# Performance work log

Measured on AMD Instinct MI355X. Metric: run time of the kernel, lower is better.

The kernel has to match this reference:

```python
import jax, jax.numpy as jnp
import numpy as np

EMBED_DIM = 1024
NUM_HEADS = 16
HEAD_DIM = EMBED_DIM // NUM_HEADS
CONSTANT = 1.0
EPS = 1e-4


def setup_inputs() -> dict:
    key = jax.random.key(0)
    ks = jax.random.split(key, 9)
    L, N, E = 2048, 4, EMBED_DIM
    scale = 1.0 / np.sqrt(E)
    return {
        "query": jax.random.normal(ks[0], (L, N, E), jnp.float32),
        "key": jax.random.normal(ks[1], (L, N, E), jnp.float32),
        "value": jax.random.normal(ks[2], (L, N, E), jnp.float32),
        "Wq": jax.random.normal(ks[3], (E, E), jnp.float32) * scale,
        "bq": jnp.zeros((E,), jnp.float32),
        "Wk": jax.random.normal(ks[4], (E, E), jnp.float32) * scale,
        "bk": jnp.zeros((E,), jnp.float32),
        "Wv": jax.random.normal(ks[5], (E, E), jnp.float32) * scale,
        "bv": jnp.zeros((E,), jnp.float32),
    }


def reference(query, key, value, Wq, bq, Wk, bk, Wv, bv):
    tgt_len, bsz, E = query.shape
    src_len = key.shape[0]
    h, d = NUM_HEADS, HEAD_DIM

    # Linear projections (nn.Linear: x @ W.T + b)
    q = query @ Wq.T + bq
    k = key @ Wk.T + bk
    v = value @ Wv.T + bv

    # (L, N, E) -> (N*h, L, d)
    def split_heads(x, slen):
        return x.reshape(slen, bsz * h, d).transpose(1, 0, 2)

    q = jax.nn.relu(split_heads(q, tgt_len))
    k = jax.nn.relu(split_heads(k, src_len))
    v = split_heads(v, src_len)

    # sin/cos positional reweighting: idx = pi/2 * arange(1, m+1) * constant / m
    m = max(src_len, tgt_len)
    idx = (np.pi / 2) * jnp.arange(1, m + 1, dtype=q.dtype) * CONSTANT / m  # (m,)
    sin_w = jnp.sin(idx)[None, :, None]  # (1, m, 1)
    cos_w = jnp.cos(idx)[None, :, None]

    q_ = jnp.concatenate([q * sin_w[:, :tgt_len], q * cos_w[:, :tgt_len]], axis=-1)  # (n, L, 2d)
    k_ = jnp.concatenate([k * sin_w[:, :src_len], k * cos_w[:, :src_len]], axis=-1)  # (n, S, 2d)

    # Non-causal linear attention: O(N) in sequence length
    kv_ = jnp.einsum('nld,nlm->ndm', k_, v)                       # (n, 2d, d)
    z_ = 1.0 / jnp.clip(jnp.einsum('nld,nd->nl', q_, k_.sum(axis=1)), EPS, None)  # (n, L)
    attn_output = jnp.einsum('nld,ndm,nl->nlm', q_, kv_, z_)      # (n, L, d)

    # (N*h, L, d) -> (L, N, E)
    attn_output = attn_output.transpose(1, 0, 2).reshape(tgt_len, bsz, E)
    return attn_output
```

## Files before the change

kernel.cpp:

```cpp
#include <hip/hip_runtime.h>
#include <cstdint>

#define L_SEQ 2048
#define NB 4
#define EMB 1024
#define NHEAD 16
#define HD 64
#define M_ROWS (L_SEQ * NB)
#define ANGC (1.5707963267948966f / 2048.0f)
#define NSPLIT 16
#define XN ((size_t)M_ROWS * EMB)
#define WN ((size_t)EMB * EMB)
#define NX16 (1 << 19)
#define NW16 (1 << 16)

typedef __bf16 bf16x8 __attribute__((ext_vector_type(8)));
typedef float f32x4 __attribute__((ext_vector_type(4)));
typedef unsigned short u16x8 __attribute__((ext_vector_type(8)));

__device__ __forceinline__ unsigned short f2bf(float f) {
  unsigned int u = __float_as_uint(f);
  u += 0x7fffu + ((u >> 16) & 1u);
  return (unsigned short)(u >> 16);
}
__device__ __forceinline__ float bf2f(unsigned short u) {
  return __uint_as_float((unsigned int)u << 16);
}

__device__ __forceinline__ void gload_lds16(const void* g, void* l) {
  __builtin_amdgcn_global_load_lds(
      (const __attribute__((address_space(1))) void*)g,
      (__attribute__((address_space(3))) void*)l, 16, 0, 0);
}

__global__ __launch_bounds__(256) void cvt_all_kernel(
    const float* __restrict__ q, const float* __restrict__ k,
    const float* __restrict__ v, const float* __restrict__ wq,
    const float* __restrict__ wk, const float* __restrict__ wv,
    unsigned short* __restrict__ xb, unsigned short* __restrict__ wb) {
  int i = blockIdx.x * 256 + threadIdx.x;
  const float* src;
  unsigned short* dst;
  size_t off;
  if (i < 3 * NX16) {
    int sel = i >> 19;
    off = (size_t)(i & (NX16 - 1));
    src = (sel == 0) ? q : (sel == 1) ? k : v;
    dst = xb + (size_t)sel * XN;
  } else {
    int j = i - 3 * NX16;
    int sel = j >> 16;
    off = (size_t)(j & (NW16 - 1));
    src = (sel == 0) ? wq : (sel == 1) ? wk : wv;
    dst = wb + (size_t)sel * WN;
  }
  const float4* s4 = (const float4*)src + off * 4;
  float4 a = s4[0], b = s4[1], c = s4[2], d = s4[3];
  union { unsigned short u[8]; uint4 vv; } o0, o1;
  o0.u[0] = f2bf(a.x); o0.u[1] = f2bf(a.y); o0.u[2] = f2bf(a.z); o0.u[3] = f2bf(a.w);
  o0.u[4] = f2bf(b.x); o0.u[5] = f2bf(b.y); o0.u[6] = f2bf(b.z); o0.u[7] = f2bf(b.w);
  o1.u[0] = f2bf(c.x); o1.u[1] = f2bf(c.y); o1.u[2] = f2bf(c.z); o1.u[3] = f2bf(c.w);
  o1.u[4] = f2bf(d.x); o1.u[5] = f2bf(d.y); o1.u[6] = f2bf(d.z); o1.u[7] = f2bf(d.w);
  uint4* d4 = (uint4*)(dst + off * 16);
  d4[0] = o0.vv;
  d4[1] = o1.vv;
}

__global__ __launch_bounds__(256) void proj_gemm_kernel(
    const unsigned short* __restrict__ Xall, const unsigned short* __restrict__ Wall,
    const float* __restrict__ b0, const float* __restrict__ b1,
    const float* __restrict__ b2, unsigned short* __restrict__ Pall) {
  const int which = blockIdx.z;
  const unsigned short* Xb = Xall + (size_t)which * XN;
  const unsigned short* Wb = Wall + (size_t)which * WN;
  const float* bias = (which == 0) ? b0 : (which == 1) ? b1 : b2;
  unsigned short* outp = Pall + (size_t)which * XN;
  const bool relu = (which < 2);
  const int bm0 = blockIdx.x * 128;
  const int bn0 = blockIdx.y * 128;

  __shared__ unsigned short As[2][128 * 32];
  __shared__ unsigned short Bs[2][128 * 32];

  const int tid = threadIdx.x;
  const int lane = tid & 63, wave = tid >> 6;
  const int wrow = (wave >> 1) * 64, wcol = (wave & 1) * 64;
  const int fr = lane & 15, fk = lane >> 4;

  f32x4 acc[4][4];
#pragma unroll
  for (int m = 0; m < 4; ++m)
#pragma unroll
    for (int n = 0; n < 4; ++n) acc[m][n] = (f32x4){0.f, 0.f, 0.f, 0.f};

  auto stage = [&](int kt, int buf) {
#pragma unroll
    for (int i = 0; i < 2; ++i) {
      int c = i * 256 + wave * 64 + lane;
      int row = c >> 2;
      int kgs = (c & 3) ^ ((row >> 1) & 3);
      int ldsoff = (i * 256 + wave * 64) * 16;
      gload_lds16(Xb + (size_t)(bm0 + row) * EMB + kt * 32 + kgs * 8,
                  (char*)&As[buf][0] + ldsoff);
      gload_lds16(Wb + (size_t)(bn0 + row) * EMB + kt * 32 + kgs * 8,
                  (char*)&Bs[buf][0] + ldsoff);
    }
  };

  stage(0, 0);
  __syncthreads();
  const int NK = EMB / 32;
  for (int kt = 0; kt < NK; ++kt) {
    int buf = kt & 1;
    if (kt + 1 < NK) stage(kt + 1, buf ^ 1);
    bf16x8 af[4], bfr[4];
#pragma unroll
    for (int m = 0; m < 4; ++m) {
      int row = wrow + m * 16 + fr;
      af[m] = *(const bf16x8*)((const char*)&As[buf][0] + row * 64 +
                               ((fk ^ ((row >> 1) & 3)) * 16));
    }
#pragma unroll
    for (int n = 0; n < 4; ++n) {
      int row = wcol + n * 16 + fr;
      bfr[n] = *(const bf16x8*)((const char*)&Bs[buf][0] + row * 64 +
                                ((fk ^ ((row >> 1) & 3)) * 16));
    }
#pragma unroll
    for (int m = 0; m < 4; ++m)
#pragma unroll
      for (int n = 0; n < 4; ++n)
        acc[m][n] = __builtin_amdgcn_mfma_f32_16x16x32_bf16(af[m], bfr[n],
                                                            acc[m][n], 0, 0, 0);
    __syncthreads();
  }

#pragma unroll
  for (int n = 0; n < 4; ++n) {
    int gc = bn0 + wcol + n * 16 + fr;
    float bv = bias[gc];
#pragma unroll
    for (int m = 0; m < 4; ++m) {
#pragma unroll
      for (int r = 0; r < 4; ++r) {
        int gr = bm0 + wrow + m * 16 + fk * 4 + r;
        float v = acc[m][n][r] + bv;
        if (relu) v = fmaxf(v, 0.f);
        outp[(size_t)gr * EMB + gc] = f2bf(v);
      }
    }
  }
}

__global__ __launch_bounds__(256) void kv_part_kernel(
    const unsigned short* __restrict__ kp, const unsigned short* __restrict__ vp,
    float* __restrict__ kvpart, float* __restrict__ kspart) {
  const int n = blockIdx.y;
  const int s = blockIdx.x;
  const int nb = n >> 4, head = n & 15;
  const int l0 = s * (L_SEQ / NSPLIT);
  __shared__ float kt[32][64];
  __shared__ float vt[32][64];
  __shared__ float wt[2][32];
  const int t = threadIdx.x;
  const int dg = t >> 3, mg = t & 7;

  float acc[4][8];
#pragma unroll
  for (int a = 0; a < 4; ++a)
#pragma unroll
    for (int b = 0; b < 8; ++b) acc[a][b] = 0.f;
  float ks[4] = {0.f, 0.f, 0.f, 0.f};

  for (int lt = l0; lt < l0 + (L_SEQ / NSPLIT); lt += 32) {
    {
      int i = t >> 3, c8 = (t & 7) * 8;
      u16x8 gk8 = *(const u16x8*)(kp + (size_t)((lt + i) * NB + nb) * EMB +
                                  head * HD + c8);
      u16x8 gv8 = *(const u16x8*)(vp + (size_t)((lt + i) * NB + nb) * EMB +
                                  head * HD + c8);
      float4 ka = {bf2f(gk8[0]), bf2f(gk8[1]), bf2f(gk8[2]), bf2f(gk8[3])};
      float4 kb = {bf2f(gk8[4]), bf2f(gk8[5]), bf2f(gk8[6]), bf2f(gk8[7])};
      float4 va = {bf2f(gv8[0]), bf2f(gv8[1]), bf2f(gv8[2]), bf2f(gv8[3])};
      float4 vb = {bf2f(gv8[4]), bf2f(gv8[5]), bf2f(gv8[6]), bf2f(gv8[7])};
      *(float4*)&kt[i][c8] = ka;
      *(float4*)&kt[i][c8 + 4] = kb;
      *(float4*)&vt[i][c8] = va;
      *(float4*)&vt[i][c8 + 4] = vb;
    }
    if (t < 32) {
      float ang = ANGC * (float)(lt + t + 1);
      wt[0][t] = __sinf(ang);
      wt[1][t] = __cosf(ang);
    }
    __syncthreads();
#pragma unroll 4
    for (int i = 0; i < 32; ++i) {
      float w = wt[dg >> 4][i];
      float4 kk4 = *(const float4*)&kt[i][(dg & 15) * 4];
      float kk[4];
      kk[0] = fmaxf(kk4.x, 0.f) * w; kk[1] = fmaxf(kk4.y, 0.f) * w;
      kk[2] = fmaxf(kk4.z, 0.f) * w; kk[3] = fmaxf(kk4.w, 0.f) * w;
      float4 v0 = *(const float4*)&vt[i][mg * 8];
      float4 v1 = *(const float4*)&vt[i][mg * 8 + 4];
      float vv[8] = {v0.x, v0.y, v0.z, v0.w, v1.x, v1.y, v1.z, v1.w};
#pragma unroll
      for (int a = 0; a < 4; ++a) {
#pragma unroll
        for (int b = 0; b < 8; ++b) acc[a][b] += kk[a] * vv[b];
        ks[a] += kk[a];
      }
    }
    __syncthreads();
  }

  float* kvn = kvpart + ((size_t)(s * 64 + n) * 128 + dg * 4) * 64 + mg * 8;
#pragma unroll
  for (int a = 0; a < 4; ++a) {
    *(float4*)&kvn[(size_t)a * 64 + 0] = *(float4*)&acc[a][0];
    *(float4*)&kvn[(size_t)a * 64 + 4] = *(float4*)&acc[a][4];
  }
  if (mg == 0) {
#pragma unroll
    for (int a = 0; a < 4; ++a)
      kspart[(size_t)(s * 64 + n) * 128 + dg * 4 + a] = ks[a];
  }
}

__global__ __launch_bounds__(256) void kv_reduce_kernel(
    const float* __restrict__ kvpart, const float* __restrict__ kspart,
    unsigned short* __restrict__ kvT, float* __restrict__ ksum) {
  const int b = blockIdx.x;
  const int n = b >> 2, mseg = b & 3;
  const int t = threadIdx.x;
  __shared__ float kvsum[128][17];

#pragma unroll
  for (int j = 0; j < 2; ++j) {
    int f4 = j * 256 + t;
    int dd = f4 >> 2, mm = f4 & 3;
    f32x4 s = (f32x4){0, 0, 0, 0};
#pragma unroll
    for (int p = 0; p < NSPLIT; ++p)
      s += *(const f32x4*)(kvpart + ((size_t)(p * 64 + n) * 128 + dd) * 64 +
                           mseg * 16 + mm * 4);
    kvsum[dd][mm * 4 + 0] = s[0];
    kvsum[dd][mm * 4 + 1] = s[1];
    kvsum[dd][mm * 4 + 2] = s[2];
    kvsum[dd][mm * 4 + 3] = s[3];
  }
  if (mseg == 0 && t < 128) {
    float s = 0.f;
#pragma unroll
    for (int p = 0; p < NSPLIT; ++p) s += kspart[(size_t)(p * 64 + n) * 128 + t];
    ksum[n * 128 + t] = s;
  }
  __syncthreads();

  int mloc = t >> 4, dd0 = (t & 15) * 8;
  union { unsigned short u[8]; uint4 vv; } o;
#pragma unroll
  for (int e = 0; e < 8; ++e) o.u[e] = f2bf(kvsum[dd0 + e][mloc]);
  *(uint4*)(kvT + ((size_t)n * 64 + mseg * 16 + mloc) * 128 + dd0) = o.vv;
}

__global__ __launch_bounds__(256) void out_mfma_kernel(
    const unsigned short* __restrict__ qp, const unsigned short* __restrict__ kvT,
    const float* __restrict__ ksum, float* __restrict__ out) {
  const int n = blockIdx.y;
  const int nb = n >> 4, head = n & 15;
  const int L0 = blockIdx.x * 64;
  const int t = threadIdx.x;
  const int lane = t & 63, wave = t >> 6;
  const int fr = lane & 15, fk = lane >> 4;

  __shared__ unsigned short q_lds[64 * 128];
  __shared__ unsigned short kvt_lds[64 * 128];
  __shared__ float ks_lds[128];
  __shared__ float z_lds[64];

  {
    int j = t >> 2, d0 = (t & 3) * 16;
    float ang = ANGC * (float)(L0 + j + 1);
    float sw = __sinf(ang), cw = __cosf(ang);
    const unsigned short* gq =
        qp + (size_t)((L0 + j) * NB + nb) * EMB + head * HD + d0;
    u16x8 qa = *(const u16x8*)gq;
    u16x8 qb = *(const u16x8*)(gq + 8);
    union { unsigned short u[8]; uint4 vv; } s0, s1, c0, c1;
#pragma unroll
    for (int e = 0; e < 8; ++e) {
      float fa = fmaxf(bf2f(qa[e]), 0.f);
      float fb = fmaxf(bf2f(qb[e]), 0.f);
      s0.u[e] = f2bf(fa * sw); s1.u[e] = f2bf(fb * sw);
      c0.u[e] = f2bf(fa * cw); c1.u[e] = f2bf(fb * cw);
    }
    int gs = (t & 3) * 2;
    *(uint4*)&q_lds[(j * 16 + ((gs + 0) ^ (j & 7))) * 8] = s0.vv;
    *(uint4*)&q_lds[(j * 16 + ((gs + 1) ^ (j & 7))) * 8] = s1.vv;
    *(uint4*)&q_lds[(j * 16 + ((gs + 8) ^ (j & 7))) * 8] = c0.vv;
    *(uint4*)&q_lds[(j * 16 + ((gs + 9) ^ (j & 7))) * 8] = c1.vv;
  }
  {
#pragma unroll
    for (int c = 0; c < 4; ++c) {
      int gi = t * 4 + c;
      int m = gi >> 4, g = gi & 15;
      uint4 v = *(const uint4*)(kvT + (size_t)n * 8192 + m * 128 + g * 8);
      *(uint4*)&kvt_lds[(m * 16 + (g ^ (m & 7))) * 8] = v;
    }
  }
  if (t < 128) ks_lds[t] = ksum[n * 128 + t];
  __syncthreads();

  {
    int row = t >> 2, seg = t & 3;
    float sum = 0.f;
#pragma unroll
    for (int g8 = 0; g8 < 4; ++g8) {
      int g = seg * 4 + g8;
      const unsigned short* qg = &q_lds[(row * 16 + (g ^ (row & 7))) * 8];
      u16x8 qv = *(const u16x8*)qg;
#pragma unroll
      for (int e = 0; e < 8; ++e) sum += bf2f(qv[e]) * ks_lds[g * 8 + e];
    }
    sum += __shfl_xor(sum, 1);
    sum += __shfl_xor(sum, 2);
    if (seg == 0) z_lds[row] = 1.f / fmaxf(sum, 1e-4f);
  }

  const int wrow = wave * 16;
  f32x4 acc[4];
#pragma unroll
  for (int nt = 0; nt < 4; ++nt) acc[nt] = (f32x4){0, 0, 0, 0};
#pragma unroll
  for (int kk = 0; kk < 4; ++kk) {
    int arow = wrow + fr;
    bf16x8 af = *(const bf16x8*)&q_lds[(arow * 16 + ((kk * 4 + fk) ^ (arow & 7))) * 8];
#pragma unroll
    for (int nt = 0; nt < 4; ++nt) {
      int brow = nt * 16 + fr;
      bf16x8 bf =
          *(const bf16x8*)&kvt_lds[(brow * 16 + ((kk * 4 + fk) ^ (brow & 7))) * 8];
      acc[nt] = __builtin_amdgcn_mfma_f32_16x16x32_bf16(af, bf, acc[nt], 0, 0, 0);
    }
  }

#pragma unroll
  for (int nt = 0; nt < 4; ++nt) {
#pragma unroll
    for (int r = 0; r < 4; ++r) {
      int lrow = wrow + fk * 4 + r;
      int m = nt * 16 + fr;
      out[((size_t)(L0 + lrow) * NB + nb) * EMB + head * HD + m] =
          acc[nt][r] * z_lds[lrow];
    }
  }
}

extern "C" void kernel_launch(void* const* d_in, const int* in_sizes, int n_in,
                              void* d_out, int out_size, void* d_ws, size_t ws_size,
                              hipStream_t stream) {
  const float* query = (const float*)d_in[0];
  const float* key = (const float*)d_in[1];
  const float* value = (const float*)d_in[2];
  const float* Wq = (const float*)d_in[3];
  const float* bq = (const float*)d_in[4];
  const float* Wk = (const float*)d_in[5];
  const float* bk = (const float*)d_in[6];
  const float* Wv = (const float*)d_in[7];
  const float* bv = (const float*)d_in[8];
  float* out = (float*)d_out;

  char* ws = (char*)d_ws;
  const size_t need = 3 * XN * 2 + 3 * WN * 2 + 3 * XN * 2 +
                      (size_t)64 * 64 * 128 * 2 + (size_t)64 * 128 * 4;
  if (ws_size < need) return;

  unsigned short* xb = (unsigned short*)ws;
  unsigned short* wb = (unsigned short*)(ws + 3 * XN * 2);
  unsigned short* proj = (unsigned short*)(ws + 3 * XN * 2 + 3 * WN * 2);
  unsigned short* kvT = (unsigned short*)(ws + 3 * XN * 2 + 3 * WN * 2 + 3 * XN * 2);
  float* ksb = (float*)(ws + 3 * XN * 2 + 3 * WN * 2 + 3 * XN * 2 +
                        (size_t)64 * 64 * 128 * 2);
  float* kvpart = (float*)ws;
  float* kspart = (float*)(ws + (size_t)NSPLIT * 64 * 128 * 64 * 4);

  const int total16 = 3 * NX16 + 3 * NW16;
  cvt_all_kernel<<<total16 / 256, 256, 0, stream>>>(query, key, value, Wq, Wk, Wv,
                                                    xb, wb);
  proj_gemm_kernel<<<dim3(64, 8, 3), 256, 0, stream>>>(xb, wb, bq, bk, bv, proj);
  kv_part_kernel<<<dim3(NSPLIT, 64), 256, 0, stream>>>(proj + 1 * XN, proj + 2 * XN,
                                                       kvpart, kspart);
  kv_reduce_kernel<<<256, 256, 0, stream>>>(kvpart, kspart, kvT, ksb);
  out_mfma_kernel<<<dim3(32, 64), 256, 0, stream>>>(proj, kvT, ksb, out);
}
```

Before: 294.1 us.

## Fuse fp32-to-bf16 activation conversion into projection GEMM A-tile loading

The separate pass that converted query/key/value activations to bf16 is removed. The projection GEMM now loads fp32 activation tiles into registers, converts them, and writes them to swizzled LDS after the MFMA work, so a full write and re-read of three large bf16 buffers is avoided. Only the weights are still pre-converted in a smaller kernel. The workspace layout is also reorganised. In exchange, each GEMM block reads twice as many A bytes (fp32), and each of the 8 column blocks re-reads and re-converts the same A tile. It also uses more registers and replaces the async global-to-LDS copy with register staging.

Result: slower. 315.5 us (+7.3%).

```diff
diff --git a/kernel.cpp b/kernel.cpp
--- a/kernel.cpp
+++ b/kernel.cpp
@@ -11,7 +11,6 @@
 #define NSPLIT 16
 #define XN ((size_t)M_ROWS * EMB)
 #define WN ((size_t)EMB * EMB)
-#define NX16 (1 << 19)
 #define NW16 (1 << 16)
 
 typedef __bf16 bf16x8 __attribute__((ext_vector_type(8)));
@@ -26,6 +25,12 @@
 __device__ __forceinline__ float bf2f(unsigned short u) {
   return __uint_as_float((unsigned int)u << 16);
 }
+__device__ __forceinline__ uint4 pack8(float4 a, float4 b) {
+  union { __bf16 h[8]; uint4 v; } o;
+  o.h[0] = (__bf16)a.x; o.h[1] = (__bf16)a.y; o.h[2] = (__bf16)a.z; o.h[3] = (__bf16)a.w;
+  o.h[4] = (__bf16)b.x; o.h[5] = (__bf16)b.y; o.h[6] = (__bf16)b.z; o.h[7] = (__bf16)b.w;
+  return o.v;
+}
 
 __device__ __forceinline__ void gload_lds16(const void* g, void* l) {
   __builtin_amdgcn_global_load_lds(
@@ -33,45 +38,28 @@
       (__attribute__((address_space(3))) void*)l, 16, 0, 0);
 }
 
-__global__ __launch_bounds__(256) void cvt_all_kernel(
-    const float* __restrict__ q, const float* __restrict__ k,
-    const float* __restrict__ v, const float* __restrict__ wq,
-    const float* __restrict__ wk, const float* __restrict__ wv,
-    unsigned short* __restrict__ xb, unsigned short* __restrict__ wb) {
+__global__ __launch_bounds__(256) void cvt_w_kernel(
+    const float* __restrict__ wq, const float* __restrict__ wk,
+    const float* __restrict__ wv, unsigned short* __restrict__ wb) {
   int i = blockIdx.x * 256 + threadIdx.x;
-  const float* src;
-  unsigned short* dst;
-  size_t off;
-  if (i < 3 * NX16) {
-    int sel = i >> 19;
-    off = (size_t)(i & (NX16 - 1));
-    src = (sel == 0) ? q : (sel == 1) ? k : v;
-    dst = xb + (size_t)sel * XN;
-  } else {
-    int j = i - 3 * NX16;
-    int sel = j >> 16;
-    off = (size_t)(j & (NW16 - 1));
-    src = (sel == 0) ? wq : (sel == 1) ? wk : wv;
-    dst = wb + (size_t)sel * WN;
-  }
+  int sel = i >> 16;
+  size_t off = (size_t)(i & (NW16 - 1));
+  const float* src = (sel == 0) ? wq : (sel == 1) ? wk : wv;
+  unsigned short* dst = wb + (size_t)sel * WN;
   const float4* s4 = (const float4*)src + off * 4;
   float4 a = s4[0], b = s4[1], c = s4[2], d = s4[3];
-  union { unsigned short u[8]; uint4 vv; } o0, o1;
-  o0.u[0] = f2bf(a.x); o0.u[1] = f2bf(a.y); o0.u[2] = f2bf(a.z); o0.u[3] = f2bf(a.w);
-  o0.u[4] = f2bf(b.x); o0.u[5] = f2bf(b.y); o0.u[6] = f2bf(b.z); o0.u[7] = f2bf(b.w);
-  o1.u[0] = f2bf(c.x); o1.u[1] = f2bf(c.y); o1.u[2] = f2bf(c.z); o1.u[3] = f2bf(c.w);
-  o1.u[4] = f2bf(d.x); o1.u[5] = f2bf(d.y); o1.u[6] = f2bf(d.z); o1.u[7] = f2bf(d.w);
   uint4* d4 = (uint4*)(dst + off * 16);
-  d4[0] = o0.vv;
-  d4[1] = o1.vv;
-}
-
-__global__ __launch_bounds__(256) void proj_gemm_kernel(
-    const unsigned short* __restrict__ Xall, const unsigned short* __restrict__ Wall,
+  d4[0] = pack8(a, b);
+  d4[1] = pack8(c, d);
+}
+
+__global__ __launch_bounds__(256) void proj_gemm_fused_kernel(
+    const float* __restrict__ Xq, const float* __restrict__ Xk,
+    const float* __restrict__ Xv, const unsigned short* __restrict__ Wall,
     const float* __restrict__ b0, const float* __restrict__ b1,
     const float* __restrict__ b2, unsigned short* __restrict__ Pall) {
   const int which = blockIdx.z;
-  const unsigned short* Xb = Xall + (size_t)which * XN;
+  const float* Xb = (which == 0) ? Xq : (which == 1) ? Xk : Xv;
   const unsigned short* Wb = Wall + (size_t)which * WN;
   const float* bias = (which == 0) ? b0 : (which == 1) ? b1 : b2;
   unsigned short* outp = Pall + (size_t)which * XN;
@@ -87,32 +75,57 @@
   const int wrow = (wave >> 1) * 64, wcol = (wave & 1) * 64;
   const int fr = lane & 15, fk = lane >> 4;
 
+  const int arow = tid >> 2, akg = tid & 3;
+
   f32x4 acc[4][4];
 #pragma unroll
   for (int m = 0; m < 4; ++m)
 #pragma unroll
     for (int n = 0; n < 4; ++n) acc[m][n] = (f32x4){0.f, 0.f, 0.f, 0.f};
 
-  auto stage = [&](int kt, int buf) {
+  auto loadA = [&](int kt, float4 r[4]) {
+    const float* src = Xb + (size_t)(bm0 + arow) * EMB + kt * 32 + akg * 8;
+    r[0] = *(const float4*)src;
+    r[1] = *(const float4*)(src + 4);
+    const float* src2 = src + (size_t)64 * EMB;
+    r[2] = *(const float4*)src2;
+    r[3] = *(const float4*)(src2 + 4);
+  };
+  auto writeA = [&](int buf, const float4 r[4]) {
+    int kgs0 = akg ^ ((arow >> 1) & 3);
+    *(uint4*)((char*)&As[buf][0] + arow * 64 + kgs0 * 16) = pack8(r[0], r[1]);
+    int row2 = arow + 64;
+    int kgs1 = akg ^ ((row2 >> 1) & 3);
+    *(uint4*)((char*)&As[buf][0] + row2 * 64 + kgs1 * 16) = pack8(r[2], r[3]);
+  };
+  auto stageB = [&](int kt, int buf) {
 #pragma unroll
     for (int i = 0; i < 2; ++i) {
       int c = i * 256 + wave * 64 + lane;
       int row = c >> 2;
       int kgs = (c & 3) ^ ((row >> 1) & 3);
       int ldsoff = (i * 256 + wave * 64) * 16;
-      gload_lds16(Xb + (size_t)(bm0 + row) * EMB + kt * 32 + kgs * 8,
-                  (char*)&As[buf][0] + ldsoff);
       gload_lds16(Wb + (size_t)(bn0 + row) * EMB + kt * 32 + kgs * 8,
                   (char*)&Bs[buf][0] + ldsoff);
     }
   };
 
-  stage(0, 0);
+  {
+    float4 ar[4];
+    loadA(0, ar);
+    stageB(0, 0);
+    writeA(0, ar);
+  }
   __syncthreads();
+
   const int NK = EMB / 32;
   for (int kt = 0; kt < NK; ++kt) {
     int buf = kt & 1;
-    if (kt + 1 < NK) stage(kt + 1, buf ^ 1);
+    float4 ar[4];
+    if (kt + 1 < NK) {
+      loadA(kt + 1, ar);
+      stageB(kt + 1, buf ^ 1);
+    }
     bf16x8 af[4], bfr[4];
 #pragma unroll
     for (int m = 0; m < 4; ++m) {
@@ -132,6 +145,7 @@
       for (int n = 0; n < 4; ++n)
         acc[m][n] = __builtin_amdgcn_mfma_f32_16x16x32_bf16(af[m], bfr[n],
                                                             acc[m][n], 0, 0, 0);
+    if (kt + 1 < NK) writeA(buf ^ 1, ar);
     __syncthreads();
   }
 
@@ -373,23 +387,25 @@
   float* out = (float*)d_out;
 
   char* ws = (char*)d_ws;
-  const size_t need = 3 * XN * 2 + 3 * WN * 2 + 3 * XN * 2 +
-                      (size_t)64 * 64 * 128 * 2 + (size_t)64 * 128 * 4;
+  const size_t wb_off = 0;
+  const size_t proj_off = 3 * WN * 2;
+  const size_t kvT_off = proj_off + 3 * XN * 2;
+  const size_t ksb_off = kvT_off + (size_t)64 * 64 * 128 * 2;
+  const size_t kvpart_off = ksb_off + (size_t)64 * 128 * 4;
+  const size_t kspart_off = kvpart_off + (size_t)NSPLIT * 64 * 128 * 64 * 4;
+  const size_t need = kspart_off + (size_t)NSPLIT * 64 * 128 * 4;
   if (ws_size < need) return;
 
-  unsigned short* xb = (unsigned short*)ws;
-  unsigned short* wb = (unsigned short*)(ws + 3 * XN * 2);
-  unsigned short* proj = (unsigned short*)(ws + 3 * XN * 2 + 3 * WN * 2);
-  unsigned short* kvT = (unsigned short*)(ws + 3 * XN * 2 + 3 * WN * 2 + 3 * XN * 2);
-  float* ksb = (float*)(ws + 3 * XN * 2 + 3 * WN * 2 + 3 * XN * 2 +
-                        (size_t)64 * 64 * 128 * 2);
-  float* kvpart = (float*)ws;
-  float* kspart = (float*)(ws + (size_t)NSPLIT * 64 * 128 * 64 * 4);
-
-  const int total16 = 3 * NX16 + 3 * NW16;
-  cvt_all_kernel<<<total16 / 256, 256, 0, stream>>>(query, key, value, Wq, Wk, Wv,
-                                                    xb, wb);
-  proj_gemm_kernel<<<dim3(64, 8, 3), 256, 0, stream>>>(xb, wb, bq, bk, bv, proj);
+  unsigned short* wb = (unsigned short*)(ws + wb_off);
+  unsigned short* proj = (unsigned short*)(ws + proj_off);
+  unsigned short* kvT = (unsigned short*)(ws + kvT_off);
+  float* ksb = (float*)(ws + ksb_off);
+  float* kvpart = (float*)(ws + kvpart_off);
+  float* kspart = (float*)(ws + kspart_off);
+
+  cvt_w_kernel<<<3 * NW16 / 256, 256, 0, stream>>>(Wq, Wk, Wv, wb);
+  proj_gemm_fused_kernel<<<dim3(64, 8, 3), 256, 0, stream>>>(
+      query, key, value, wb, bq, bk, bv, proj);
   kv_part_kernel<<<dim3(NSPLIT, 64), 256, 0, stream>>>(proj + 1 * XN, proj + 2 * XN,
                                                        kvpart, kspart);
   kv_reduce_kernel<<<256, 256, 0, stream>>>(kvpart, kspart, kvT, ksb);
```
